# Performance work log

Hardware: AMD Instinct MI355X
Metric: run time of the kernel (lower is better)

Reference implementation:

```python
import jax, jax.numpy as jnp
import numpy as np

D_MODEL = 1024
HEADS = 16
D_K = D_MODEL // HEADS


def setup_inputs() -> dict:
    key = jax.random.key(0)
    ks = jax.random.split(key, 11)
    B, S = 4, 2048
    scale = 1.0 / np.sqrt(D_MODEL)
    return {
        "q": jax.random.normal(ks[0], (B, S, D_MODEL), jnp.float32),
        "k": jax.random.normal(ks[1], (B, S, D_MODEL), jnp.float32),
        "v": jax.random.normal(ks[2], (B, S, D_MODEL), jnp.float32),
        "wq": jax.random.normal(ks[3], (D_MODEL, D_MODEL), jnp.float32) * scale,
        "bq": jax.random.normal(ks[4], (D_MODEL,), jnp.float32) * 0.01,
        "wk": jax.random.normal(ks[5], (D_MODEL, D_MODEL), jnp.float32) * scale,
        "bk": jax.random.normal(ks[6], (D_MODEL,), jnp.float32) * 0.01,
        "wv": jax.random.normal(ks[7], (D_MODEL, D_MODEL), jnp.float32) * scale,
        "bv": jax.random.normal(ks[8], (D_MODEL,), jnp.float32) * 0.01,
        "wo": jax.random.normal(ks[9], (D_MODEL, D_MODEL), jnp.float32) * scale,
        "bo": jax.random.normal(ks[10], (D_MODEL,), jnp.float32) * 0.01,
    }


def reference(q, k, v, wq, bq, wk, bk, wv, bv, wo, bo):
    B, S, _ = q.shape
    # nn.Linear: x @ W^T + b
    qp = q @ wq.T + bq
    kp = k @ wk.T + bk
    vp = v @ wv.T + bv
    # [B, S, D] -> [B, H, S, d_k]
    def split_heads(x):
        return x.reshape(B, S, HEADS, D_K).transpose(0, 2, 1, 3)
    qh, kh, vh = split_heads(qp), split_heads(kp), split_heads(vp)
    # scaled dot-product attention (dropout p=0 -> identity)
    scores = jnp.einsum("bhsd,bhtd->bhst", qh, kh) / jnp.sqrt(jnp.float32(D_K)).astype(qh.dtype)
    attn = jax.nn.softmax(scores, axis=-1)
    ctx = jnp.einsum("bhst,bhtd->bhsd", attn, vh)
    # merge heads and output projection
    ctx = ctx.transpose(0, 2, 1, 3).reshape(B, S, D_MODEL)
    return ctx @ wo.T + bo
```

## Files before the change

### kernel.cpp

```cpp
#include <hip/hip_runtime.h>


typedef __attribute__((ext_vector_type(8))) short bf16x8;
typedef __attribute__((ext_vector_type(4))) float f32x4;
typedef unsigned int u32;

#define DEVI __device__ __forceinline__

static constexpr int S_LEN = 2048;
static constexpr int NH = 16;
static constexpr int DK = 64;
static constexpr float Q_SCALE = 0.125f * 1.44269504088896340736f;

DEVI unsigned short f2b(float f) {
    unsigned int u = __builtin_bit_cast(unsigned int, f);
    u += 0x7fffu + ((u >> 16) & 1u);
    return (unsigned short)(u >> 16);
}

DEVI u32 pkbf16(float a, float b) {
#if __has_builtin(__builtin_amdgcn_cvt_pk_bf16_f32)
    auto r = __builtin_amdgcn_cvt_pk_bf16_f32(a, b);
    return __builtin_bit_cast(u32, r);
#else
    return (u32)f2b(a) | ((u32)f2b(b) << 16);
#endif
}

DEVI float fexp2(float x) {
#if __has_builtin(__builtin_amdgcn_exp2f)
    return __builtin_amdgcn_exp2f(x);
#else
    return exp2f(x);
#endif
}

DEVI f32x4 mfma16(bf16x8 a, bf16x8 b, f32x4 c) {
    return __builtin_amdgcn_mfma_f32_16x16x32_bf16(a, b, c, 0, 0, 0);
}

#define GLL16(g, l)                                                        \
    __builtin_amdgcn_global_load_lds(                                      \
        (const __attribute__((address_space(1))) u32*)(g),                 \
        (__attribute__((address_space(3))) u32*)(l), 16, 0, 0)

#define SBAR __builtin_amdgcn_sched_barrier(0)
#define PHB  SBAR; __builtin_amdgcn_s_barrier(); SBAR

__global__ __launch_bounds__(256) void cvt3(
    const float* __restrict__ q, const float* __restrict__ k,
    const float* __restrict__ v, unsigned short* __restrict__ dq,
    unsigned short* __restrict__ dk, unsigned short* __restrict__ dv) {
    const int z = blockIdx.y;
    const float* src = z == 0 ? q : z == 1 ? k : v;
    unsigned short* dst = z == 0 ? dq : z == 1 ? dk : dv;
    long i = ((long)blockIdx.x * 256 + threadIdx.x) * 8;
    float4 v0 = *(const float4*)(src + i);
    float4 v1 = *(const float4*)(src + i + 4);
    uint4 o;
    o.x = pkbf16(v0.x, v0.y);
    o.y = pkbf16(v0.z, v0.w);
    o.z = pkbf16(v1.x, v1.y);
    o.w = pkbf16(v1.z, v1.w);
    *(uint4*)(dst + i) = o;
}

__global__ __launch_bounds__(256) void cvt_w(
    const float* __restrict__ a, const float* __restrict__ b,
    const float* __restrict__ c, const float* __restrict__ d,
    unsigned short* __restrict__ o) {
    const float* src = blockIdx.y == 0 ? a : blockIdx.y == 1 ? b
                     : blockIdx.y == 2 ? c : d;
    unsigned short* dst = o + (long)blockIdx.y * 1048576;
    long i = ((long)blockIdx.x * 256 + threadIdx.x) * 8;
    float4 v0 = *(const float4*)(src + i);
    float4 v1 = *(const float4*)(src + i + 4);
    uint4 ov;
    ov.x = pkbf16(v0.x, v0.y);
    ov.y = pkbf16(v0.z, v0.w);
    ov.z = pkbf16(v1.x, v1.y);
    ov.w = pkbf16(v1.z, v1.w);
    *(uint4*)(dst + i) = ov;
}

#define MM8(MH, NH, BB)                                                    \
    __builtin_amdgcn_s_setprio(1);                                         \
    _Pragma("unroll") for (int mi = 0; mi < 4; ++mi)                       \
        _Pragma("unroll") for (int ni = 0; ni < 2; ++ni)                   \
            _Pragma("unroll") for (int kk = 0; kk < 2; ++kk)               \
                acc[(MH)*4 + mi][(NH)*2 + ni] = mfma16(                    \
                    a[mi][kk], BB[ni][kk], acc[(MH)*4 + mi][(NH)*2 + ni]); \
    __builtin_amdgcn_s_setprio(0);

DEVI void gemm256_core(const unsigned short* __restrict__ Am,
                       const unsigned short* __restrict__ Wm,
                       int m0, int n0, int tid, f32x4 (&acc)[8][4]) {
    __shared__ __align__(16) unsigned short As[2][256 * 64];
    __shared__ __align__(16) unsigned short Bs[2][256 * 64];
    const int wid = tid >> 6, l = tid & 63, l16 = l & 15, quad = l >> 4;
    const int swz = l16 & 7;
    const int wm = (wid >> 2) * 128, wn = (wid & 3) * 64;
    unsigned short *As0 = &As[0][0], *As1 = &As[1][0];
    unsigned short *Bs0 = &Bs[0][0], *Bs1 = &Bs[1][0];

    bf16x8 a[4][2], b0[2][2], b1[2][2];

    auto stg = [&](const unsigned short* Mat, int r0, int ko,
                   unsigned short* lds, int type) {
        #pragma unroll
        for (int pass = 0; pass < 2; ++pass) {
            int wlr = pass * 64 + wid * 8;
            int row0 = type == 0 ? (wlr < 64 ? wlr : wlr + 64)
                     : type == 1 ? 64 + (wlr < 64 ? wlr : wlr + 64)
                     : type == 2 ? (wlr & 31) + (wlr >> 5) * 64
                                 : 32 + (wlr & 31) + (wlr >> 5) * 64;
            int row = row0 + (l >> 3);
            int cl = (l & 7) ^ (l >> 3);
            GLL16(Mat + (long)(r0 + row) * 1024 + ko + cl * 8, lds + row0 * 64);
        }
    };
    auto lda = [&](const unsigned short* as, int mh) {
        #pragma unroll
        for (int mi = 0; mi < 4; ++mi)
            #pragma unroll
            for (int kk = 0; kk < 2; ++kk)
                a[mi][kk] = *(const bf16x8*)(as +
                    (wm + (mh * 4 + mi) * 16 + l16) * 64 +
                    (((kk * 4 + quad) ^ swz) << 3));
    };
    auto ldb = [&](const unsigned short* bs, int nh, bf16x8 (&bb)[2][2]) {
        #pragma unroll
        for (int ni = 0; ni < 2; ++ni)
            #pragma unroll
            for (int kk = 0; kk < 2; ++kk)
                bb[ni][kk] = *(const bf16x8*)(bs +
                    (wn + (nh * 2 + ni) * 16 + l16) * 64 +
                    (((kk * 4 + quad) ^ swz) << 3));
    };

    stg(Am, m0, 0, As0, 0); stg(Wm, n0, 0, Bs0, 2);
    stg(Wm, n0, 0, Bs0, 3); stg(Am, m0, 0, As0, 1);
    stg(Am, m0, 64, As1, 0); stg(Wm, n0, 64, Bs1, 2); stg(Wm, n0, 64, Bs1, 3);
    asm volatile("s_waitcnt vmcnt(6)" ::: "memory");
    __builtin_amdgcn_s_barrier(); SBAR;

    #pragma unroll 1
    for (int it = 0; it < 8; ++it) {
        const bool F = it < 7;
        const int ko1 = it * 128 + 64, ko2 = it * 128 + 128, ko3 = it * 128 + 192;
        lda(As0, 0); ldb(Bs0, 0, b0);
        stg(Am, m0, ko1, As1, 1);
        PHB; MM8(0, 0, b0); PHB;
        ldb(Bs0, 1, b1);
        if (F) stg(Am, m0, ko2, As0, 0);
        PHB; MM8(0, 1, b1); PHB;
        lda(As0, 1);
        if (F) stg(Wm, n0, ko2, Bs0, 2);
        PHB; MM8(1, 0, b0); PHB;
        if (F) stg(Wm, n0, ko2, Bs0, 3);
        PHB; MM8(1, 1, b1);
        SBAR;
        if (F) { asm volatile("s_waitcnt vmcnt(6)" ::: "memory"); }
        else   { asm volatile("s_waitcnt vmcnt(0)" ::: "memory"); }
        __builtin_amdgcn_s_barrier(); SBAR;
        lda(As1, 0); ldb(Bs1, 0, b0);
        if (F) stg(Am, m0, ko2, As0, 1);
        PHB; MM8(0, 0, b0); PHB;
        ldb(Bs1, 1, b1);
        if (F) stg(Am, m0, ko3, As1, 0);
        PHB; MM8(0, 1, b1); PHB;
        lda(As1, 1);
        if (F) stg(Wm, n0, ko3, Bs1, 2);
        PHB; MM8(1, 0, b0); PHB;
        if (F) stg(Wm, n0, ko3, Bs1, 3);
        PHB; MM8(1, 1, b1);
        SBAR;
        if (F) { asm volatile("s_waitcnt vmcnt(6)" ::: "memory"); }
        __builtin_amdgcn_s_barrier(); SBAR;
    }
}

__global__ __launch_bounds__(512, 2) void gemm_qkv(
    const unsigned short* __restrict__ aq, const unsigned short* __restrict__ ak,
    const unsigned short* __restrict__ av, const unsigned short* __restrict__ wqkv,
    const float* __restrict__ bq, const float* __restrict__ bk,
    const float* __restrict__ bv, unsigned short* __restrict__ qh,
    unsigned short* __restrict__ kh, unsigned short* __restrict__ vht) {
    const int tid = threadIdx.x;
    const int wid = tid >> 6, l = tid & 63, l16 = l & 15, quad = l >> 4;
    const int wm = (wid >> 2) * 128, wn = (wid & 3) * 64;
    const int m0 = blockIdx.y * 256, n0 = blockIdx.x * 256;
    const int z = blockIdx.z;
    const unsigned short* Am = z == 0 ? aq : z == 1 ? ak : av;
    const unsigned short* Wm = wqkv + (long)z * 1048576;
    const float* bias = z == 0 ? bq : z == 1 ? bk : bv;

    f32x4 acc[8][4] = {};
    gemm256_core(Am, Wm, m0, n0, tid, acc);

    if (z < 2) {
        unsigned short* out = z == 0 ? qh : kh;
        const float scale = z == 0 ? Q_SCALE : 1.0f;
        #pragma unroll
        for (int ni = 0; ni < 4; ++ni) {
            int n = n0 + wn + ni * 16 + l16;
            float bvl = bias[n];
            int hh = n >> 6, dd = n & 63;
            #pragma unroll
            for (int mi = 0; mi < 8; ++mi)
                #pragma unroll
                for (int r = 0; r < 4; ++r) {
                    int m = m0 + wm + mi * 16 + quad * 4 + r;
                    int bb = m >> 11, ss = m & 2047;
                    out[(((long)(bb * NH + hh) * S_LEN + ss) * DK) + dd] =
                        f2b((acc[mi][ni][r] + bvl) * scale);
                }
        }
    } else {
        #pragma unroll
        for (int ni = 0; ni < 4; ++ni) {
            int n = n0 + wn + ni * 16 + l16;
            float bvl = bias[n];
            int hh = n >> 6, dd = n & 63;
            #pragma unroll
            for (int mi = 0; mi < 8; ++mi) {
                int m = m0 + wm + mi * 16 + quad * 4;
                int bb = m >> 11, ss = m & 2047;
                uint2 pk;
                pk.x = pkbf16(acc[mi][ni][0] + bvl, acc[mi][ni][1] + bvl);
                pk.y = pkbf16(acc[mi][ni][2] + bvl, acc[mi][ni][3] + bvl);
                *(uint2*)(vht + ((long)(bb * NH + hh) * DK + dd) * S_LEN + ss) = pk;
            }
        }
    }
}

__global__ __launch_bounds__(512, 2) void gemm_out(
    const unsigned short* __restrict__ A, const unsigned short* __restrict__ W,
    const float* __restrict__ bias, float* __restrict__ out) {
    const int tid = threadIdx.x;
    const int wid = tid >> 6, l = tid & 63, l16 = l & 15, quad = l >> 4;
    const int wm = (wid >> 2) * 128, wn = (wid & 3) * 64;
    const int m0 = blockIdx.y * 256, n0 = blockIdx.x * 256;

    f32x4 acc[8][4] = {};
    gemm256_core(A, W, m0, n0, tid, acc);

    #pragma unroll
    for (int ni = 0; ni < 4; ++ni) {
        int n = n0 + wn + ni * 16 + l16;
        float bv = bias[n];
        #pragma unroll
        for (int mi = 0; mi < 8; ++mi)
            #pragma unroll
            for (int r = 0; r < 4; ++r) {
                int m = m0 + wm + mi * 16 + quad * 4 + r;
                out[(long)m * 1024 + n] = acc[mi][ni][r] + bv;
            }
    }
}

__global__ __launch_bounds__(256, 3) void attn(
    const unsigned short* __restrict__ qh, const unsigned short* __restrict__ kh,
    const unsigned short* __restrict__ vht, unsigned short* __restrict__ ctx) {
    __shared__ __align__(16) unsigned short Kb[2][4096];
    __shared__ __align__(16) unsigned short Vb[3][4096];
    __shared__ __align__(16) unsigned short P[128 * 44];

    const int id = blockIdx.y * 16 + blockIdx.x;
    const int id2 = (id & 7) * 128 + (id >> 3);
    const int qt = id2 & 15, bh = id2 >> 4;
    const int tid = threadIdx.x;
    const int w = tid >> 6, l = tid & 63, l16 = l & 15, quad = l >> 4;

    const unsigned short* kh_b = kh + (long)bh * 2048 * 64;
    const unsigned short* vh_b = vht + (long)bh * 64 * 2048;

    const unsigned short* qsrc = qh + ((long)bh * 2048 + qt * 128) * 64;
    bf16x8 qf[2][2];
    #pragma unroll
    for (int dd = 0; dd < 2; ++dd)
        #pragma unroll
        for (int i = 0; i < 2; ++i)
            qf[dd][i] = *(const bf16x8*)(qsrc + (w * 32 + i * 16 + l16) * 64 +
                                         dd * 32 + quad * 8);
    #pragma unroll
    for (int dd = 0; dd < 2; ++dd)
        #pragma unroll
        for (int i = 0; i < 2; ++i)
            asm volatile("" :: "v"(qf[dd][i]));

    auto stage_k = [&](const unsigned short* base, int buf) {
        #pragma unroll
        for (int rr = 0; rr < 2; ++rr) {
            int sb = rr * 256 + w * 64;
            int slot = sb + l;
            int row = slot >> 3, cc = (slot & 7) ^ (row & 7);
            GLL16(base + (long)row * 64 + cc * 8, &Kb[buf][sb * 8]);
        }
    };
    auto stage_v = [&](const unsigned short* vbase, int buf) {
        #pragma unroll
        for (int rr = 0; rr < 2; ++rr) {
            int sb = rr * 256 + w * 64;
            int slot = sb + l;
            int d = slot >> 3, cc = (slot & 7) ^ (d & 7);
            GLL16(vbase + (long)d * 2048 + cc * 8, &Vb[buf][sb * 8]);
        }
    };

    stage_k(kh_b, 0);
    stage_v(vh_b, 0);
    stage_v(vh_b + 64, 1);
    asm volatile("s_waitcnt vmcnt(2)" ::: "memory");
    __builtin_amdgcn_s_barrier();
    __builtin_amdgcn_sched_barrier(0);

    f32x4 o[4][2] = {};
    f32x4 osum[2] = {};
    bf16x8 ones;
    #pragma unroll
    for (int j = 0; j < 8; ++j) ones[j] = (short)0x3f80;

    const unsigned short* kstage = kh_b + 64 * 64;
    const unsigned short* vstage = vh_b + 2 * 64;
    int vr = 0, vs = 2;
    for (int kt = 0; kt < 32; ++kt) {
        if (kt < 31) stage_k(kstage, (kt + 1) & 1);
        if (kt < 30) stage_v(vstage, vs);
        kstage += 64 * 64;
        vstage += 64;
        __builtin_amdgcn_sched_barrier(0);

        const unsigned short* kb = Kb[kt & 1];
        f32x4 sa[2][4] = {};
        #pragma unroll
        for (int dd = 0; dd < 2; ++dd) {
            bf16x8 kf[4];
            #pragma unroll
            for (int ja = 0; ja < 4; ++ja) {
                int row = ja * 16 + l16;
                kf[ja] = *(const bf16x8*)(kb + (row * 8 + ((dd * 4 + quad) ^ (row & 7))) * 8);
            }
            __builtin_amdgcn_s_setprio(1);
            #pragma unroll
            for (int i = 0; i < 2; ++i)
                #pragma unroll
                for (int ja = 0; ja < 4; ++ja)
                    sa[i][ja] = mfma16(kf[ja], qf[dd][i], sa[i][ja]);
            __builtin_amdgcn_s_setprio(0);
        }

        #pragma unroll
        for (int i = 0; i < 2; ++i)
            #pragma unroll
            for (int ja = 0; ja < 4; ++ja)
                #pragma unroll
                for (int r = 0; r < 4; ++r)
                    sa[i][ja][r] = fexp2(sa[i][ja][r]);

        const unsigned short* vb = Vb[vr];
        #pragma unroll
        for (int qtr = 0; qtr < 2; ++qtr) {
            #pragma unroll
            for (int jh = 0; jh < 2; ++jh)
                #pragma unroll
                for (int i = 0; i < 2; ++i) {
                    int row = w * 32 + i * 16 + l16;
                    int ja = qtr * 2 + jh;
                    uint2 pk;
                    pk.x = pkbf16(sa[i][ja][0], sa[i][ja][1]);
                    pk.y = pkbf16(sa[i][ja][2], sa[i][ja][3]);
                    *(uint2*)(&P[row * 44 + jh * 16 + quad * 4]) = pk;
                }
            bf16x8 vf[4], pf[2];
            #pragma unroll
            for (int jd = 0; jd < 4; ++jd) {
                int d = jd * 16 + l16;
                vf[jd] = *(const bf16x8*)(vb + (d * 8 + ((qtr * 4 + quad) ^ (d & 7))) * 8);
            }
            #pragma unroll
            for (int i = 0; i < 2; ++i) {
                int row = w * 32 + i * 16 + l16;
                pf[i] = *(const bf16x8*)(&P[row * 44 + quad * 8]);
            }
            __builtin_amdgcn_s_setprio(1);
            #pragma unroll
            for (int jd = 0; jd < 4; ++jd)
                #pragma unroll
                for (int i = 0; i < 2; ++i)
                    o[jd][i] = mfma16(vf[jd], pf[i], o[jd][i]);
            #pragma unroll
            for (int i = 0; i < 2; ++i)
                osum[i] = mfma16(ones, pf[i], osum[i]);
            __builtin_amdgcn_s_setprio(0);
        }

        if (kt < 30) {
            asm volatile("s_waitcnt vmcnt(2)" ::: "memory");
        } else if (kt == 30) {
            asm volatile("s_waitcnt vmcnt(0)" ::: "memory");
        }
        if (kt < 31) {
            __builtin_amdgcn_s_barrier();
            __builtin_amdgcn_sched_barrier(0);
        }

        vr = (vr + 1 == 3) ? 0 : vr + 1;
        vs = (vs + 1 == 3) ? 0 : vs + 1;
    }

    const int b = bh >> 4, hh = bh & 15;
    #pragma unroll
    for (int i = 0; i < 2; ++i) {
        float inv = 1.0f / osum[i][0];
        int s = qt * 128 + w * 32 + i * 16 + l16;
        #pragma unroll
        for (int jd = 0; jd < 4; ++jd) {
            uint2 pk;
            pk.x = pkbf16(o[jd][i][0] * inv, o[jd][i][1] * inv);
            pk.y = pkbf16(o[jd][i][2] * inv, o[jd][i][3] * inv);
            *(uint2*)(&ctx[((long)(b * 2048 + s) * 1024) + hh * 64 + jd * 16 + quad * 4]) = pk;
        }
    }
}

extern "C" void kernel_launch(void* const* d_in, const int* in_sizes, int n_in,
                              void* d_out, int out_size, void* d_ws, size_t ws_size,
                              hipStream_t stream) {
    const float* q  = (const float*)d_in[0];
    const float* k  = (const float*)d_in[1];
    const float* v  = (const float*)d_in[2];
    const float* wq = (const float*)d_in[3];
    const float* bq = (const float*)d_in[4];
    const float* wk = (const float*)d_in[5];
    const float* bk = (const float*)d_in[6];
    const float* wv = (const float*)d_in[7];
    const float* bv = (const float*)d_in[8];
    const float* wo = (const float*)d_in[9];
    const float* bo = (const float*)d_in[10];
    float* out = (float*)d_out;

    const size_t NE = 8u * 1024u * 1024u;
    unsigned short* ab_q = (unsigned short*)d_ws;
    unsigned short* qh   = ab_q + NE;
    unsigned short* kh   = qh + NE;
    unsigned short* vht  = kh + NE;
    unsigned short* wb   = vht + NE;
    unsigned short* wob  = wb + 3 * 1048576;
    unsigned short* ctx  = ab_q;
    unsigned short* ab_k = (unsigned short*)d_out;
    unsigned short* ab_v = ab_k + NE;

    cvt_w<<<dim3(512, 4), dim3(256), 0, stream>>>(wq, wk, wv, wo, wb);
    cvt3<<<dim3(4096, 3), dim3(256), 0, stream>>>(q, k, v, ab_q, ab_k, ab_v);
    gemm_qkv<<<dim3(4, 32, 3), dim3(512), 0, stream>>>(ab_q, ab_k, ab_v, wb,
                                                       bq, bk, bv, qh, kh, vht);
    attn<<<dim3(16, 64), dim3(256), 0, stream>>>(qh, kh, vht, ctx);
    gemm_out<<<dim3(4, 32), dim3(512), 0, stream>>>(ctx, wob, bo, out);
}
```

Measured before the change: 365.5 us.

## Shrink GEMM tiles to 256x128, remap block order, fuse conversion kernels

The projection GEMMs move from 256x256 to 256x128 output tiles, doubling the grid. The MFMA/load schedule is restructured with a single B fragment set and a new vmcnt budget. A block-index remap groups blocks that share the same A rows, and the two fp32-to-bf16 conversion kernels are merged into one launch. The aim is better CU occupancy (gemm_out had only 128 blocks for 256 CUs) and one fewer launch, at the cost of lower arithmetic intensity per tile and more A-matrix reloads.

```diff
diff --git a/kernel.cpp b/kernel.cpp
--- a/kernel.cpp
+++ b/kernel.cpp
@@ -47,14 +47,29 @@
 #define SBAR __builtin_amdgcn_sched_barrier(0)
 #define PHB  SBAR; __builtin_amdgcn_s_barrier(); SBAR
 
-__global__ __launch_bounds__(256) void cvt3(
+__global__ __launch_bounds__(256) void cvt_all(
     const float* __restrict__ q, const float* __restrict__ k,
-    const float* __restrict__ v, unsigned short* __restrict__ dq,
-    unsigned short* __restrict__ dk, unsigned short* __restrict__ dv) {
-    const int z = blockIdx.y;
-    const float* src = z == 0 ? q : z == 1 ? k : v;
-    unsigned short* dst = z == 0 ? dq : z == 1 ? dk : dv;
-    long i = ((long)blockIdx.x * 256 + threadIdx.x) * 8;
+    const float* __restrict__ v, const float* __restrict__ wq,
+    const float* __restrict__ wk, const float* __restrict__ wv,
+    const float* __restrict__ wo, unsigned short* __restrict__ dq,
+    unsigned short* __restrict__ dk, unsigned short* __restrict__ dv,
+    unsigned short* __restrict__ wb) {
+    const int id = blockIdx.x;
+    const float* src;
+    unsigned short* dst;
+    long i;
+    if (id < 12288) {
+        int z = id >> 12, x = id & 4095;
+        src = z == 0 ? q : z == 1 ? k : v;
+        dst = z == 0 ? dq : z == 1 ? dk : dv;
+        i = ((long)x * 256 + threadIdx.x) * 8;
+    } else {
+        int wi = id - 12288;
+        int z = wi >> 9, x = wi & 511;
+        src = z == 0 ? wq : z == 1 ? wk : z == 2 ? wv : wo;
+        dst = wb + (long)z * 1048576;
+        i = ((long)x * 256 + threadIdx.x) * 8;
+    }
     float4 v0 = *(const float4*)(src + i);
     float4 v1 = *(const float4*)(src + i + 4);
     uint4 o;
@@ -65,45 +80,27 @@
     *(uint4*)(dst + i) = o;
 }
 
-__global__ __launch_bounds__(256) void cvt_w(
-    const float* __restrict__ a, const float* __restrict__ b,
-    const float* __restrict__ c, const float* __restrict__ d,
-    unsigned short* __restrict__ o) {
-    const float* src = blockIdx.y == 0 ? a : blockIdx.y == 1 ? b
-                     : blockIdx.y == 2 ? c : d;
-    unsigned short* dst = o + (long)blockIdx.y * 1048576;
-    long i = ((long)blockIdx.x * 256 + threadIdx.x) * 8;
-    float4 v0 = *(const float4*)(src + i);
-    float4 v1 = *(const float4*)(src + i + 4);
-    uint4 ov;
-    ov.x = pkbf16(v0.x, v0.y);
-    ov.y = pkbf16(v0.z, v0.w);
-    ov.z = pkbf16(v1.x, v1.y);
-    ov.w = pkbf16(v1.z, v1.w);
-    *(uint4*)(dst + i) = ov;
-}
-
-#define MM8(MH, NH, BB)                                                    \
+#define MM16(MH)                                                           \
     __builtin_amdgcn_s_setprio(1);                                         \
     _Pragma("unroll") for (int mi = 0; mi < 4; ++mi)                       \
         _Pragma("unroll") for (int ni = 0; ni < 2; ++ni)                   \
             _Pragma("unroll") for (int kk = 0; kk < 2; ++kk)               \
-                acc[(MH)*4 + mi][(NH)*2 + ni] = mfma16(                    \
-                    a[mi][kk], BB[ni][kk], acc[(MH)*4 + mi][(NH)*2 + ni]); \
+                acc[(MH)*4 + mi][ni] = mfma16(                             \
+                    a[mi][kk], b[ni][kk], acc[(MH)*4 + mi][ni]);           \
     __builtin_amdgcn_s_setprio(0);
 
-DEVI void gemm256_core(const unsigned short* __restrict__ Am,
-                       const unsigned short* __restrict__ Wm,
-                       int m0, int n0, int tid, f32x4 (&acc)[8][4]) {
+DEVI void gemm_core(const unsigned short* __restrict__ Am,
+                    const unsigned short* __restrict__ Wm,
+                    int m0, int n0, int tid, f32x4 (&acc)[8][2]) {
     __shared__ __align__(16) unsigned short As[2][256 * 64];
-    __shared__ __align__(16) unsigned short Bs[2][256 * 64];
+    __shared__ __align__(16) unsigned short Bs[2][128 * 64];
     const int wid = tid >> 6, l = tid & 63, l16 = l & 15, quad = l >> 4;
     const int swz = l16 & 7;
-    const int wm = (wid >> 2) * 128, wn = (wid & 3) * 64;
+    const int wm = (wid >> 2) * 128, wn = (wid & 3) * 32;
     unsigned short *As0 = &As[0][0], *As1 = &As[1][0];
     unsigned short *Bs0 = &Bs[0][0], *Bs1 = &Bs[1][0];
 
-    bf16x8 a[4][2], b0[2][2], b1[2][2];
+    bf16x8 a[4][2], b[2][2];
 
     auto stg = [&](const unsigned short* Mat, int r0, int ko,
                    unsigned short* lds, int type) {
@@ -112,8 +109,7 @@
             int wlr = pass * 64 + wid * 8;
             int row0 = type == 0 ? (wlr < 64 ? wlr : wlr + 64)
                      : type == 1 ? 64 + (wlr < 64 ? wlr : wlr + 64)
-                     : type == 2 ? (wlr & 31) + (wlr >> 5) * 64
-                                 : 32 + (wlr & 31) + (wlr >> 5) * 64;
+                                 : wlr;
             int row = row0 + (l >> 3);
             int cl = (l & 7) ^ (l >> 3);
             GLL16(Mat + (long)(r0 + row) * 1024 + ko + cl * 8, lds + row0 * 64);
@@ -128,56 +124,55 @@
                     (wm + (mh * 4 + mi) * 16 + l16) * 64 +
                     (((kk * 4 + quad) ^ swz) << 3));
     };
-    auto ldb = [&](const unsigned short* bs, int nh, bf16x8 (&bb)[2][2]) {
+    auto ldb = [&](const unsigned short* bs) {
         #pragma unroll
         for (int ni = 0; ni < 2; ++ni)
             #pragma unroll
             for (int kk = 0; kk < 2; ++kk)
-                bb[ni][kk] = *(const bf16x8*)(bs +
-                    (wn + (nh * 2 + ni) * 16 + l16) * 64 +
+                b[ni][kk] = *(const bf16x8*)(bs +
+                    (wn + ni * 16 + l16) * 64 +
                     (((kk * 4 + quad) ^ swz) << 3));
     };
 
-    stg(Am, m0, 0, As0, 0); stg(Wm, n0, 0, Bs0, 2);
-    stg(Wm, n0, 0, Bs0, 3); stg(Am, m0, 0, As0, 1);
-    stg(Am, m0, 64, As1, 0); stg(Wm, n0, 64, Bs1, 2); stg(Wm, n0, 64, Bs1, 3);
-    asm volatile("s_waitcnt vmcnt(6)" ::: "memory");
+    stg(Am, m0, 0, As0, 0);
+    stg(Wm, n0, 0, Bs0, 2);
+    stg(Am, m0, 0, As0, 1);
+    stg(Am, m0, 64, As1, 0);
+    asm volatile("s_waitcnt vmcnt(2)" ::: "memory");
     __builtin_amdgcn_s_barrier(); SBAR;
 
     #pragma unroll 1
     for (int it = 0; it < 8; ++it) {
         const bool F = it < 7;
         const int ko1 = it * 128 + 64, ko2 = it * 128 + 128, ko3 = it * 128 + 192;
-        lda(As0, 0); ldb(Bs0, 0, b0);
+        lda(As0, 0); ldb(Bs0);
+        stg(Wm, n0, ko1, Bs1, 2);
         stg(Am, m0, ko1, As1, 1);
-        PHB; MM8(0, 0, b0); PHB;
-        ldb(Bs0, 1, b1);
+        PHB; MM16(0); PHB;
+        lda(As0, 1);
         if (F) stg(Am, m0, ko2, As0, 0);
-        PHB; MM8(0, 1, b1); PHB;
-        lda(As0, 1);
-        if (F) stg(Wm, n0, ko2, Bs0, 2);
-        PHB; MM8(1, 0, b0); PHB;
-        if (F) stg(Wm, n0, ko2, Bs0, 3);
-        PHB; MM8(1, 1, b1);
+        PHB; MM16(1);
         SBAR;
-        if (F) { asm volatile("s_waitcnt vmcnt(6)" ::: "memory"); }
+        if (F) { asm volatile("s_waitcnt vmcnt(2)" ::: "memory"); }
         else   { asm volatile("s_waitcnt vmcnt(0)" ::: "memory"); }
         __builtin_amdgcn_s_barrier(); SBAR;
-        lda(As1, 0); ldb(Bs1, 0, b0);
-        if (F) stg(Am, m0, ko2, As0, 1);
-        PHB; MM8(0, 0, b0); PHB;
-        ldb(Bs1, 1, b1);
+        lda(As1, 0); ldb(Bs1);
+        if (F) { stg(Wm, n0, ko2, Bs0, 2); stg(Am, m0, ko2, As0, 1); }
+        PHB; MM16(0); PHB;
+        lda(As1, 1);
         if (F) stg(Am, m0, ko3, As1, 0);
-        PHB; MM8(0, 1, b1); PHB;
-        lda(As1, 1);
-        if (F) stg(Wm, n0, ko3, Bs1, 2);
-        PHB; MM8(1, 0, b0); PHB;
-        if (F) stg(Wm, n0, ko3, Bs1, 3);
-        PHB; MM8(1, 1, b1);
+        PHB; MM16(1);
         SBAR;
-        if (F) { asm volatile("s_waitcnt vmcnt(6)" ::: "memory"); }
+        if (F) { asm volatile("s_waitcnt vmcnt(2)" ::: "memory"); }
         __builtin_amdgcn_s_barrier(); SBAR;
     }
+}
+
+DEVI void gemm_bid(int& m0, int& n0) {
+    int bid = blockIdx.y * 8 + blockIdx.x;
+    int b2 = (bid & 7) * 32 + (bid >> 3);
+    m0 = (b2 >> 3) * 256;
+    n0 = (b2 & 7) * 128;
 }
 
 __global__ __launch_bounds__(512, 2) void gemm_qkv(
@@ -188,21 +183,22 @@
     unsigned short* __restrict__ kh, unsigned short* __restrict__ vht) {
     const int tid = threadIdx.x;
     const int wid = tid >> 6, l = tid & 63, l16 = l & 15, quad = l >> 4;
-    const int wm = (wid >> 2) * 128, wn = (wid & 3) * 64;
-    const int m0 = blockIdx.y * 256, n0 = blockIdx.x * 256;
+    const int wm = (wid >> 2) * 128, wn = (wid & 3) * 32;
+    int m0, n0;
+    gemm_bid(m0, n0);
     const int z = blockIdx.z;
     const unsigned short* Am = z == 0 ? aq : z == 1 ? ak : av;
     const unsigned short* Wm = wqkv + (long)z * 1048576;
     const float* bias = z == 0 ? bq : z == 1 ? bk : bv;
 
-    f32x4 acc[8][4] = {};
-    gemm256_core(Am, Wm, m0, n0, tid, acc);
+    f32x4 acc[8][2] = {};
+    gemm_core(Am, Wm, m0, n0, tid, acc);
 
     if (z < 2) {
         unsigned short* out = z == 0 ? qh : kh;
         const float scale = z == 0 ? Q_SCALE : 1.0f;
         #pragma unroll
-        for (int ni = 0; ni < 4; ++ni) {
+        for (int ni = 0; ni < 2; ++ni) {
             int n = n0 + wn + ni * 16 + l16;
             float bvl = bias[n];
             int hh = n >> 6, dd = n & 63;
@@ -218,7 +214,7 @@
         }
     } else {
         #pragma unroll
-        for (int ni = 0; ni < 4; ++ni) {
+        for (int ni = 0; ni < 2; ++ni) {
             int n = n0 + wn + ni * 16 + l16;
             float bvl = bias[n];
             int hh = n >> 6, dd = n & 63;
@@ -240,14 +236,15 @@
     const float* __restrict__ bias, float* __restrict__ out) {
     const int tid = threadIdx.x;
     const int wid = tid >> 6, l = tid & 63, l16 = l & 15, quad = l >> 4;
-    const int wm = (wid >> 2) * 128, wn = (wid & 3) * 64;
-    const int m0 = blockIdx.y * 256, n0 = blockIdx.x * 256;
-
-    f32x4 acc[8][4] = {};
-    gemm256_core(A, W, m0, n0, tid, acc);
+    const int wm = (wid >> 2) * 128, wn = (wid & 3) * 32;
+    int m0, n0;
+    gemm_bid(m0, n0);
+
+    f32x4 acc[8][2] = {};
+    gemm_core(A, W, m0, n0, tid, acc);
 
     #pragma unroll
-    for (int ni = 0; ni < 4; ++ni) {
+    for (int ni = 0; ni < 2; ++ni) {
         int n = n0 + wn + ni * 16 + l16;
         float bv = bias[n];
         #pragma unroll
@@ -452,10 +449,10 @@
     unsigned short* ab_k = (unsigned short*)d_out;
     unsigned short* ab_v = ab_k + NE;
 
-    cvt_w<<<dim3(512, 4), dim3(256), 0, stream>>>(wq, wk, wv, wo, wb);
-    cvt3<<<dim3(4096, 3), dim3(256), 0, stream>>>(q, k, v, ab_q, ab_k, ab_v);
-    gemm_qkv<<<dim3(4, 32, 3), dim3(512), 0, stream>>>(ab_q, ab_k, ab_v, wb,
+    cvt_all<<<dim3(14336), dim3(256), 0, stream>>>(q, k, v, wq, wk, wv, wo,
+                                                   ab_q, ab_k, ab_v, wb);
+    gemm_qkv<<<dim3(8, 32, 3), dim3(512), 0, stream>>>(ab_q, ab_k, ab_v, wb,
                                                        bq, bk, bv, qh, kh, vht);
     attn<<<dim3(16, 64), dim3(256), 0, stream>>>(qh, kh, vht, ctx);
-    gemm_out<<<dim3(4, 32), dim3(512), 0, stream>>>(ctx, wob, bo, out);
-}
+    gemm_out<<<dim3(8, 32), dim3(512), 0, stream>>>(ctx, wob, bo, out);
+}
```

Result: faster. 345.7 us (-5.4%).
